# Kernel optimization log

Hardware: AMD Instinct MI355X
Metric: run time of the kernel (lower is better)

Reference implementation:

```python
import jax, jax.numpy as jnp
import numpy as np

N_QUBITS = 10
QLCU_LAYERS = 2
FEATURE_DIM = 256
BATCH = 256
N_PARAMS = 5 * N_QUBITS * QLCU_LAYERS  # 100
TWO_PI = 2.0 * np.pi


def _rx_mat(theta):
    # (B,) -> (B,2,2) complex64
    c = jnp.cos(theta / 2).astype(jnp.complex64)
    s = (-1j * jnp.sin(theta / 2)).astype(jnp.complex64)
    return jnp.stack([jnp.stack([c, s], -1), jnp.stack([s, c], -1)], -2)


def _ry_mat(theta):
    c = jnp.cos(theta / 2).astype(jnp.complex64)
    s = jnp.sin(theta / 2).astype(jnp.complex64)
    return jnp.stack([jnp.stack([c, -s], -1), jnp.stack([s, c], -1)], -2)


def _rz_mat(theta):
    e0 = jnp.exp(-0.5j * theta.astype(jnp.complex64))
    e1 = jnp.exp(0.5j * theta.astype(jnp.complex64))
    z = jnp.zeros_like(e0)
    return jnp.stack([jnp.stack([e0, z], -1), jnp.stack([z, e1], -1)], -2)


def _apply_1q(state, U, w):
    # state: (B,)+(2,)*n ; U: (B,2,2) ; wire w (PennyLane wire 0 = most significant)
    s = jnp.moveaxis(state, 1 + w, -1)
    s = jnp.einsum('bij,b...j->b...i', U, s)
    return jnp.moveaxis(s, -1, 1 + w)


def _apply_crx(state, theta, c, t):
    # controlled-RX: apply RX(theta) on target t where control c == 1
    s = jnp.moveaxis(state, (1 + c, 1 + t), (-2, -1))
    U = _rx_mat(theta)
    s1 = jnp.einsum('bij,b...j->b...i', U, s[..., 1, :])
    s = jnp.stack([s[..., 0, :], s1], axis=-2)
    return jnp.moveaxis(s, (-2, -1), (1 + c, 1 + t))


def _circuit(params):
    # params: (B, N_PARAMS) angles. Returns (B, 3*n) expvals [X.., Y.., Z..]
    n = N_QUBITS
    B = params.shape[0]
    state = jnp.zeros((B,) + (2,) * n, jnp.complex64)
    state = state.at[(slice(None),) + (0,) * n].set(1.0)
    idx = 0
    for _ in range(QLCU_LAYERS):
        for i in range(n):
            state = _apply_1q(state, _rx_mat(params[:, idx]), i)
            state = _apply_1q(state, _ry_mat(params[:, idx + 1]), i)
            state = _apply_1q(state, _rz_mat(params[:, idx + 2]), i)
            idx += 3
        for i in range(n):
            state = _apply_crx(state, params[:, idx], i, (i + 1) % n)
            idx += 1
        for i in range(n - 1, -1, -1):
            state = _apply_crx(state, params[:, idx], i, (i - 1) % n)
            idx += 1
    X, Y, Z = [], [], []
    for w in range(n):
        s = jnp.moveaxis(state, 1 + w, -1).reshape(B, -1, 2)
        z01 = jnp.sum(jnp.conj(s[..., 0]) * s[..., 1], axis=1)  # (B,)
        X.append(2.0 * jnp.real(z01))
        Y.append(2.0 * jnp.imag(z01))
        probs = jnp.sum(jnp.abs(s) ** 2, axis=1)  # (B,2)
        Z.append(probs[:, 0] - probs[:, 1])
    return jnp.stack(X + Y + Z, axis=1).astype(jnp.float32)


def _branch(x, W, b, base):
    p = x @ W.T + b            # (B, N_PARAMS)
    p = p + base[None, :]
    p = jax.nn.sigmoid(p) * TWO_PI
    return _circuit(p)


def setup_inputs() -> dict:
    key = jax.random.key(0)
    ks = jax.random.split(key, 16)
    d = {
        'x': jax.random.normal(ks[0], (BATCH, FEATURE_DIM), jnp.float32),
        'W1': jax.random.normal(ks[1], (N_PARAMS, FEATURE_DIM), jnp.float32) * 0.05,
        'b1': jnp.zeros((N_PARAMS,), jnp.float32),
        'W2': jax.random.normal(ks[2], (N_PARAMS, FEATURE_DIM), jnp.float32) * 0.05,
        'b2': jnp.zeros((N_PARAMS,), jnp.float32),
        'W3': jax.random.normal(ks[3], (N_PARAMS, FEATURE_DIM), jnp.float32) * 0.05,
        'b3': jnp.zeros((N_PARAMS,), jnp.float32),
        'base1': jax.random.uniform(ks[4], (N_PARAMS,), jnp.float32) * TWO_PI,
        'base2': jax.random.uniform(ks[5], (N_PARAMS,), jnp.float32) * TWO_PI,
        'base3': jax.random.uniform(ks[6], (N_PARAMS,), jnp.float32) * TWO_PI,
        'alpha_real': jax.random.uniform(ks[7], (1,), jnp.float32),
        'alpha_imag': jnp.zeros((1,), jnp.float32),
        'beta_real': jax.random.uniform(ks[8], (1,), jnp.float32),
        'beta_imag': jnp.zeros((1,), jnp.float32),
        'gamma_real': jax.random.uniform(ks[9], (1,), jnp.float32),
        'gamma_imag': jnp.zeros((1,), jnp.float32),
    }
    return d


def reference(x, W1, b1, W2, b2, W3, b3, base1, base2, base3,
              alpha_real, alpha_imag, beta_real, beta_imag, gamma_real, gamma_imag):
    m1 = _branch(x, W1, b1, base1)  # (B, 3n)
    m2 = _branch(x, W2, b2, base2)
    m3 = _branch(x, W3, b3, base3)
    norm = jnp.sqrt(alpha_real**2 + alpha_imag**2 + beta_real**2 + beta_imag**2
                    + gamma_real**2 + gamma_imag**2 + 1e-9)
    ar, ai = alpha_real / norm, alpha_imag / norm
    br, bi = beta_real / norm, beta_imag / norm
    gr, gi = gamma_real / norm, gamma_imag / norm
    re = ar * m1 + br * m2 + gr * m3
    im = ai * m1 + bi * m2 + gi * m3
    return jnp.sqrt(re * re + im * im)
```

## Files before the change

kernel.cpp:

```cpp
#include <hip/hip_runtime.h>
#include <math.h>

#define NQ 10
#define NPAR 100
#define FDIM 256
#define BATCH 256
#define NOUT 30
#define TWO_PI_F 6.283185307179586f
#define NSLOT 4


template<int MASK>
__device__ __forceinline__ float lx(float v) {
    if constexpr (MASK == 1) {
        return __int_as_float(__builtin_amdgcn_update_dpp(
            0, __float_as_int(v), 0xB1, 0xF, 0xF, true));
    } else if constexpr (MASK == 2) {
        return __int_as_float(__builtin_amdgcn_update_dpp(
            0, __float_as_int(v), 0x4E, 0xF, 0xF, true));
    } else if constexpr (MASK == 8) {
        return __int_as_float(__builtin_amdgcn_update_dpp(
            0, __float_as_int(v), 0x128, 0xF, 0xF, true));
    } else if constexpr (MASK == 4) {
        return __int_as_float(__builtin_amdgcn_ds_swizzle(__float_as_int(v), 0x101F));
    } else if constexpr (MASK == 16) {
        return __int_as_float(__builtin_amdgcn_ds_swizzle(__float_as_int(v), 0x401F));
    } else {
        return __shfl_xor(v, 32, 64);
    }
}

template<int MASK>
__device__ __forceinline__ float2 lx2(float2 v) {
    return make_float2(lx<MASK>(v.x), lx<MASK>(v.y));
}

__device__ __forceinline__ float2 cmul(float2 a, float2 b) {
    return make_float2(a.x*b.x - a.y*b.y, a.x*b.y + a.y*b.x);
}

struct Ctx {
    int lane;
    int W;
    int ebuf;
    float2 (*ex)[4][NSLOT][64];
};

template<int BC, int BT>
__device__ __forceinline__ void crx(float2 (&st)[NSLOT], Ctx& cx, float c, float s)
{
    if constexpr (BT >= 8) {
        constexpr int tb = BT - 8;
        const int PW = cx.W ^ (1 << tb);
        if constexpr (BC >= 8) {
            const bool ctrl = (cx.W >> (BC - 8)) & 1;
            if (ctrl) {
                #pragma unroll
                for (int a = 0; a < NSLOT; ++a) cx.ex[cx.ebuf][cx.W][a][cx.lane] = st[a];
            }
            __syncthreads();
            if (ctrl) {
                #pragma unroll
                for (int a = 0; a < NSLOT; ++a) {
                    const float2 p = cx.ex[cx.ebuf][PW][a][cx.lane];
                    const float2 m = st[a];
                    st[a] = make_float2(c*m.x + s*p.y, c*m.y - s*p.x);
                }
            }
            cx.ebuf ^= 1;
        } else if constexpr (BC >= 6) {
            constexpr int rc = 1 << (BC - 6);
            #pragma unroll
            for (int a = 0; a < NSLOT; ++a) if (a & rc) cx.ex[cx.ebuf][cx.W][a][cx.lane] = st[a];
            __syncthreads();
            #pragma unroll
            for (int a = 0; a < NSLOT; ++a) if (a & rc) {
                const float2 p = cx.ex[cx.ebuf][PW][a][cx.lane];
                const float2 m = st[a];
                st[a] = make_float2(c*m.x + s*p.y, c*m.y - s*p.x);
            }
            cx.ebuf ^= 1;
        } else {
            #pragma unroll
            for (int a = 0; a < NSLOT; ++a) cx.ex[cx.ebuf][cx.W][a][cx.lane] = st[a];
            __syncthreads();
            const bool act = (cx.lane >> BC) & 1;
            const float cc = act ? c : 1.f, ss = act ? s : 0.f;
            #pragma unroll
            for (int a = 0; a < NSLOT; ++a) {
                const float2 p = cx.ex[cx.ebuf][PW][a][cx.lane];
                const float2 m = st[a];
                st[a] = make_float2(cc*m.x + ss*p.y, cc*m.y - ss*p.x);
            }
            cx.ebuf ^= 1;
        }
    } else if constexpr (BC >= 8) {
        const bool ctrl = (cx.W >> (BC - 8)) & 1;
        if (ctrl) {
            if constexpr (BT >= 6) {
                constexpr int rt = 1 << (BT - 6);
                #pragma unroll
                for (int a = 0; a < NSLOT; ++a) {
                    if (a & rt) continue;
                    const int a1 = a | rt;
                    const float2 A0 = st[a], A1 = st[a1];
                    st[a]  = make_float2(c*A0.x + s*A1.y, c*A0.y - s*A1.x);
                    st[a1] = make_float2(c*A1.x + s*A0.y, c*A1.y - s*A0.x);
                }
            } else {
                constexpr int M = 1 << BT;
                #pragma unroll
                for (int a = 0; a < NSLOT; ++a) {
                    const float2 p = lx2<M>(st[a]); const float2 m = st[a];
                    st[a] = make_float2(c*m.x + s*p.y, c*m.y - s*p.x);
                }
            }
        }
    } else if constexpr (BT >= 6) {
        constexpr int rt = 1 << (BT - 6);
        if constexpr (BC >= 6) {
            constexpr int rc = 1 << (BC - 6);
            #pragma unroll
            for (int a = 0; a < NSLOT; ++a) {
                if (!(a & rc) || (a & rt)) continue;
                const int a1 = a | rt;
                const float2 A0 = st[a], A1 = st[a1];
                st[a]  = make_float2(c*A0.x + s*A1.y, c*A0.y - s*A1.x);
                st[a1] = make_float2(c*A1.x + s*A0.y, c*A1.y - s*A0.x);
            }
        } else {
            const bool act = (cx.lane >> BC) & 1;
            const float cc = act ? c : 1.f, ss = act ? s : 0.f;
            #pragma unroll
            for (int a = 0; a < NSLOT; ++a) {
                if (a & rt) continue;
                const int a1 = a | rt;
                const float2 A0 = st[a], A1 = st[a1];
                st[a]  = make_float2(cc*A0.x + ss*A1.y, cc*A0.y - ss*A1.x);
                st[a1] = make_float2(cc*A1.x + ss*A0.y, cc*A1.y - ss*A0.x);
            }
        }
    } else {
        constexpr int M = 1 << BT;
        if constexpr (BC >= 6) {
            constexpr int rc = 1 << (BC - 6);
            #pragma unroll
            for (int a = 0; a < NSLOT; ++a) {
                if (!(a & rc)) continue;
                const float2 p = lx2<M>(st[a]); const float2 m = st[a];
                st[a] = make_float2(c*m.x + s*p.y, c*m.y - s*p.x);
            }
        } else {
            const bool act = (cx.lane >> BC) & 1;
            const float cc = act ? c : 1.f, ss = act ? s : 0.f;
            #pragma unroll
            for (int a = 0; a < NSLOT; ++a) {
                const float2 p = lx2<M>(st[a]); const float2 m = st[a];
                st[a] = make_float2(cc*m.x + ss*p.y, cc*m.y - ss*p.x);
            }
        }
    }
}

template<int BIT>
__device__ __forceinline__ void gate1q(float2 (&st)[NSLOT], Ctx& cx,
                                       float2 u00, float2 u01, float2 u10, float2 u11)
{
    if constexpr (BIT >= 8) {
        constexpr int tb = BIT - 8;
        const int PW = cx.W ^ (1 << tb);
        #pragma unroll
        for (int a = 0; a < NSLOT; ++a) cx.ex[cx.ebuf][cx.W][a][cx.lane] = st[a];
        __syncthreads();
        const bool hi = (cx.W >> tb) & 1;
        const float2 A = hi ? u11 : u00;
        const float2 B = hi ? u10 : u01;
        #pragma unroll
        for (int a = 0; a < NSLOT; ++a) {
            const float2 m = st[a];
            const float2 p = cx.ex[cx.ebuf][PW][a][cx.lane];
            st[a] = make_float2(A.x*m.x - A.y*m.y + B.x*p.x - B.y*p.y,
                                A.x*m.y + A.y*m.x + B.x*p.y + B.y*p.x);
        }
        cx.ebuf ^= 1;
    } else if constexpr (BIT >= 6) {
        constexpr int rb = 1 << (BIT - 6);
        #pragma unroll
        for (int a = 0; a < NSLOT; ++a) {
            if (a & rb) continue;
            const int a1 = a | rb;
            const float2 A0 = st[a], A1 = st[a1];
            float2 n0, n1;
            n0.x = u00.x*A0.x - u00.y*A0.y + u01.x*A1.x - u01.y*A1.y;
            n0.y = u00.x*A0.y + u00.y*A0.x + u01.x*A1.y + u01.y*A1.x;
            n1.x = u10.x*A0.x - u10.y*A0.y + u11.x*A1.x - u11.y*A1.y;
            n1.y = u10.x*A0.y + u10.y*A0.x + u11.x*A1.y + u11.y*A1.x;
            st[a] = n0; st[a1] = n1;
        }
    } else {
        constexpr int M = 1 << BIT;
        const bool hi = (cx.lane >> BIT) & 1;
        const float2 A = hi ? u11 : u00;
        const float2 B = hi ? u10 : u01;
        #pragma unroll
        for (int a = 0; a < NSLOT; ++a) {
            const float2 p = lx2<M>(st[a]); const float2 m = st[a];
            st[a] = make_float2(A.x*m.x - A.y*m.y + B.x*p.x - B.y*p.y,
                                A.x*m.y + A.y*m.x + B.x*p.y + B.y*p.x);
        }
    }
}

template<int Q>
__device__ __forceinline__ void layer1q(float2 (&st)[NSLOT], Ctx& cx,
                                        const float2* cs, int idx)
{
    if constexpr (Q < NQ) {
        const float2 X = cs[idx], Y = cs[idx + 1], Z = cs[idx + 2];
        const float cx_ = X.x, sx = X.y, cy = Y.x, sy = Y.y, cz = Z.x, sz = Z.y;
        const float2 m00 = make_float2( cy*cx_,  sy*sx);
        const float2 m01 = make_float2(-sy*cx_, -cy*sx);
        const float2 m10 = make_float2( sy*cx_, -cy*sx);
        const float2 m11 = make_float2( cy*cx_, -sy*sx);
        const float2 u00 = make_float2(cz*m00.x + sz*m00.y, cz*m00.y - sz*m00.x);
        const float2 u01 = make_float2(cz*m01.x + sz*m01.y, cz*m01.y - sz*m01.x);
        const float2 u10 = make_float2(cz*m10.x - sz*m10.y, cz*m10.y + sz*m10.x);
        const float2 u11 = make_float2(cz*m11.x - sz*m11.y, cz*m11.y + sz*m11.x);
        gate1q<9 - Q>(st, cx, u00, u01, u10, u11);
        layer1q<Q + 1>(st, cx, cs, idx + 3);
    }
}

template<int Q>
__device__ __forceinline__ void ringF(float2 (&st)[NSLOT], Ctx& cx,
                                      const float2* cs, int idx)
{
    if constexpr (Q < NQ) {
        const float2 p = cs[idx];
        crx<9 - Q, 9 - ((Q + 1) % NQ)>(st, cx, p.x, p.y);
        ringF<Q + 1>(st, cx, cs, idx + 1);
    }
}

template<int Q>
__device__ __forceinline__ void ringB(float2 (&st)[NSLOT], Ctx& cx,
                                      const float2* cs, int idx)
{
    if constexpr (Q >= 0) {
        const float2 p = cs[idx];
        crx<9 - Q, 9 - ((Q + NQ - 1) % NQ)>(st, cx, p.x, p.y);
        ringB<Q - 1>(st, cx, cs, idx + 1);
    }
}

__device__ __forceinline__ void col0(const float2* cs, int w, float2& u00, float2& u10)
{
    const float2 X = cs[3*w], Y = cs[3*w + 1], Z = cs[3*w + 2];
    const float cx = X.x, sx = X.y, cy = Y.x, sy = Y.y, cz = Z.x, sz = Z.y;
    const float2 m00 = make_float2(cy*cx,  sy*sx);
    const float2 m10 = make_float2(sy*cx, -cy*sx);
    u00 = make_float2(cz*m00.x + sz*m00.y, cz*m00.y - sz*m00.x);
    u10 = make_float2(cz*m10.x - sz*m10.y, cz*m10.y + sz*m10.x);
}

template<int Wq>
__device__ __forceinline__ void measureAll(const float2 (&st)[NSLOT], Ctx& cx,
                                           float* mrow )
{
    if constexpr (Wq < NQ) {
        constexpr int B = 9 - Wq;
        float sre = 0.f, smm = 0.f, szz = 0.f;
        if constexpr (B >= 8) {
            constexpr int tb = B - 8;
            const int PW = cx.W ^ (1 << tb);
            #pragma unroll
            for (int a = 0; a < NSLOT; ++a) cx.ex[cx.ebuf][cx.W][a][cx.lane] = st[a];
            __syncthreads();
            const float sgn = ((cx.W >> tb) & 1) ? -1.f : 1.f;
            #pragma unroll
            for (int a = 0; a < NSLOT; ++a) {
                const float2 m = st[a];
                const float2 p = cx.ex[cx.ebuf][PW][a][cx.lane];
                sre += m.x*p.x + m.y*p.y;
                smm += sgn * (m.x*p.y - m.y*p.x);
                szz += sgn * (m.x*m.x + m.y*m.y);
            }
            cx.ebuf ^= 1;
        } else if constexpr (B >= 6) {
            constexpr int rb = 1 << (B - 6);
            #pragma unroll
            for (int a = 0; a < NSLOT; ++a) {
                if (a & rb) continue;
                const int a1 = a | rb;
                const float2 A0 = st[a], A1 = st[a1];
                sre += A0.x*A1.x + A0.y*A1.y;
                smm += A0.x*A1.y - A0.y*A1.x;
                szz += A0.x*A0.x + A0.y*A0.y - A1.x*A1.x - A1.y*A1.y;
            }
            sre *= 2.f; smm *= 2.f;
        } else {
            constexpr int M = 1 << B;
            const float sgn = ((cx.lane >> B) & 1) ? -1.f : 1.f;
            #pragma unroll
            for (int a = 0; a < NSLOT; ++a) {
                const float2 m = st[a];
                const float2 p = lx2<M>(m);
                sre += m.x*p.x + m.y*p.y;
                smm += sgn * (m.x*p.y - m.y*p.x);
                szz += sgn * (m.x*m.x + m.y*m.y - p.x*p.x - p.y*p.y);
            }
            szz *= 0.5f;
        }
        sre += lx<1>(sre); sre += lx<2>(sre); sre += lx<4>(sre); sre += lx<8>(sre); sre += lx<16>(sre);
        smm += lx<1>(smm); smm += lx<2>(smm); smm += lx<4>(smm); smm += lx<8>(smm); smm += lx<16>(smm);
        szz += lx<1>(szz); szz += lx<2>(szz); szz += lx<4>(szz); szz += lx<8>(szz); szz += lx<16>(szz);
        if ((cx.lane & 31) == 0) {
            const int k = (cx.W << 1) | (cx.lane >> 5);
            mrow[k * NOUT + Wq]      = sre;
            mrow[k * NOUT + 10 + Wq] = smm;
            mrow[k * NOUT + 20 + Wq] = szz;
        }
        measureAll<Wq + 1>(st, cx, mrow);
    }
}

__global__ __launch_bounds__(768) void qsb_fused(
    const float* __restrict__ x,
    const float* __restrict__ W1, const float* __restrict__ b1, const float* __restrict__ base1,
    const float* __restrict__ W2, const float* __restrict__ b2, const float* __restrict__ base2,
    const float* __restrict__ W3, const float* __restrict__ b3, const float* __restrict__ base3,
    const float* __restrict__ ar_, const float* __restrict__ ai_,
    const float* __restrict__ br_, const float* __restrict__ bi_,
    const float* __restrict__ gr_, const float* __restrict__ gi_,
    float* __restrict__ out)
{
    const int tid  = threadIdx.x;
    const int b    = blockIdx.x;
    const int wv   = tid >> 6;
    const int br   = wv >> 2;
    const int W    = wv & 3;
    const int lane = tid & 63;
    const int lt   = (W << 6) | lane;

    const float* Wp   = (br == 0) ? W1    : (br == 1) ? W2    : W3;
    const float* bias = (br == 0) ? b1    : (br == 1) ? b2    : b3;
    const float* base = (br == 0) ? base1 : (br == 1) ? base2 : base3;

    __shared__ float2 css[3][NPAR];
    __shared__ float2 exb[3][2][4][NSLOT][64];
    __shared__ float  mred[3][8][NOUT];

    if (lt < NPAR) {
        const float4* xr = reinterpret_cast<const float4*>(x + (size_t)b * FDIM);
        const float4* wr = reinterpret_cast<const float4*>(Wp + (size_t)lt * FDIM);
        float a0 = 0.f, a1 = 0.f, a2 = 0.f, a3 = 0.f;
        #pragma unroll 8
        for (int k = 0; k < FDIM / 4; ++k) {
            const float4 xv = xr[k];
            const float4 wv4 = wr[k];
            a0 += xv.x*wv4.x; a1 += xv.y*wv4.y; a2 += xv.z*wv4.z; a3 += xv.w*wv4.w;
        }
        float acc = (a0 + a1) + (a2 + a3);
        acc += bias[lt] + base[lt];
        const float t = TWO_PI_F / (1.f + __expf(-acc));
        float sn, cn;
        __sincosf(0.5f * t, &sn, &cn);
        css[br][lt] = make_float2(cn, sn);
    }
    __syncthreads();

    const float2* cs = css[br];
    Ctx cx;
    cx.lane = lane; cx.W = W; cx.ebuf = 0;
    cx.ex = exb[br];

    float2 st[NSLOT];
    {
        float2 lp = make_float2(1.f, 0.f);
        #pragma unroll
        for (int bb = 0; bb < 6; ++bb) {
            float2 u00, u10;
            col0(cs, 9 - bb, u00, u10);
            lp = cmul(lp, ((lane >> bb) & 1) ? u10 : u00);
        }
        {
            float2 u00, u10;
            col0(cs, 1, u00, u10);
            lp = cmul(lp, (W & 1) ? u10 : u00);
        }
        {
            float2 u00, u10;
            col0(cs, 0, u00, u10);
            lp = cmul(lp, ((W >> 1) & 1) ? u10 : u00);
        }
        float2 f3[2], f2v[2];
        col0(cs, 3, f3[0], f3[1]);
        col0(cs, 2, f2v[0], f2v[1]);
        #pragma unroll
        for (int a = 0; a < NSLOT; ++a)
            st[a] = cmul(cmul(f3[a & 1], f2v[(a >> 1) & 1]), lp);
    }

    ringF<0>(st, cx, cs, 30);
    ringB<NQ - 1>(st, cx, cs, 40);
    layer1q<0>(st, cx, cs, 50);
    ringF<0>(st, cx, cs, 80);
    ringB<NQ - 1>(st, cx, cs, 90);

    measureAll<0>(st, cx, &mred[br][0][0]);
    __syncthreads();

    if (tid < NOUT) {
        const int j = tid;
        float m1 = 0.f, m2 = 0.f, m3 = 0.f;
        #pragma unroll
        for (int k = 0; k < 8; ++k) {
            m1 += mred[0][k][j];
            m2 += mred[1][k][j];
            m3 += mred[2][k][j];
        }
        const float ar = ar_[0], ai = ai_[0];
        const float brr = br_[0], bii = bi_[0];
        const float gr = gr_[0], gi = gi_[0];
        const float inv = 1.f / sqrtf(ar*ar + ai*ai + brr*brr + bii*bii
                                      + gr*gr + gi*gi + 1e-9f);
        const float re = (ar * m1 + brr * m2 + gr * m3) * inv;
        const float im = (ai * m1 + bii * m2 + gi * m3) * inv;
        out[(size_t)b * NOUT + j] = sqrtf(re * re + im * im);
    }
}

extern "C" void kernel_launch(void* const* d_in, const int* in_sizes, int n_in,
                              void* d_out, int out_size, void* d_ws, size_t ws_size,
                              hipStream_t stream)
{
    (void)in_sizes; (void)n_in; (void)out_size; (void)d_ws; (void)ws_size;
    const float* x     = (const float*)d_in[0];
    const float* W1    = (const float*)d_in[1];
    const float* b1    = (const float*)d_in[2];
    const float* W2    = (const float*)d_in[3];
    const float* b2    = (const float*)d_in[4];
    const float* W3    = (const float*)d_in[5];
    const float* b3    = (const float*)d_in[6];
    const float* base1 = (const float*)d_in[7];
    const float* base2 = (const float*)d_in[8];
    const float* base3 = (const float*)d_in[9];
    const float* ar    = (const float*)d_in[10];
    const float* ai    = (const float*)d_in[11];
    const float* br    = (const float*)d_in[12];
    const float* bi    = (const float*)d_in[13];
    const float* gr    = (const float*)d_in[14];
    const float* gi    = (const float*)d_in[15];

    qsb_fused<<<dim3(BATCH), dim3(768), 0, stream>>>(
        x, W1, b1, base1, W2, b2, base2, W3, b3, base3,
        ar, ai, br, bi, gr, gi, (float*)d_out);
}
```

Baseline: 107.2 us.

## Split fused kernel into per-branch simulation blocks plus a combine kernel

The single 768-thread block per sample, which ran all three branch circuits, becomes three 256-thread blocks per sample, one per branch. Each writes its partial expectation values to workspace, and a second small kernel applies the complex weighting and magnitude. The aim is finer-grained blocks that schedule better across CUs and allow higher occupancy. The cost is an extra kernel launch and a global-memory round trip for the partials.

```diff
diff --git a/kernel.cpp b/kernel.cpp
--- a/kernel.cpp
+++ b/kernel.cpp
@@ -324,35 +324,31 @@
     }
 }
 
-__global__ __launch_bounds__(768) void qsb_fused(
+__global__ __launch_bounds__(256) void qsb_sim(
     const float* __restrict__ x,
     const float* __restrict__ W1, const float* __restrict__ b1, const float* __restrict__ base1,
     const float* __restrict__ W2, const float* __restrict__ b2, const float* __restrict__ base2,
     const float* __restrict__ W3, const float* __restrict__ b3, const float* __restrict__ base3,
-    const float* __restrict__ ar_, const float* __restrict__ ai_,
-    const float* __restrict__ br_, const float* __restrict__ bi_,
-    const float* __restrict__ gr_, const float* __restrict__ gi_,
-    float* __restrict__ out)
-{
+    float* __restrict__ gpart )
+{
+    const int bb   = blockIdx.x;
+    const int b    = bb / 3;
+    const int br   = bb - 3 * b;
     const int tid  = threadIdx.x;
-    const int b    = blockIdx.x;
-    const int wv   = tid >> 6;
-    const int br   = wv >> 2;
-    const int W    = wv & 3;
+    const int W    = tid >> 6;
     const int lane = tid & 63;
-    const int lt   = (W << 6) | lane;
 
     const float* Wp   = (br == 0) ? W1    : (br == 1) ? W2    : W3;
     const float* bias = (br == 0) ? b1    : (br == 1) ? b2    : b3;
     const float* base = (br == 0) ? base1 : (br == 1) ? base2 : base3;
 
-    __shared__ float2 css[3][NPAR];
-    __shared__ float2 exb[3][2][4][NSLOT][64];
-    __shared__ float  mred[3][8][NOUT];
-
-    if (lt < NPAR) {
+    __shared__ float2 css[NPAR];
+    __shared__ float2 exb[2][4][NSLOT][64];
+    __shared__ float  mred[8][NOUT];
+
+    if (tid < NPAR) {
         const float4* xr = reinterpret_cast<const float4*>(x + (size_t)b * FDIM);
-        const float4* wr = reinterpret_cast<const float4*>(Wp + (size_t)lt * FDIM);
+        const float4* wr = reinterpret_cast<const float4*>(Wp + (size_t)tid * FDIM);
         float a0 = 0.f, a1 = 0.f, a2 = 0.f, a3 = 0.f;
         #pragma unroll 8
         for (int k = 0; k < FDIM / 4; ++k) {
@@ -361,27 +357,27 @@
             a0 += xv.x*wv4.x; a1 += xv.y*wv4.y; a2 += xv.z*wv4.z; a3 += xv.w*wv4.w;
         }
         float acc = (a0 + a1) + (a2 + a3);
-        acc += bias[lt] + base[lt];
+        acc += bias[tid] + base[tid];
         const float t = TWO_PI_F / (1.f + __expf(-acc));
         float sn, cn;
         __sincosf(0.5f * t, &sn, &cn);
-        css[br][lt] = make_float2(cn, sn);
+        css[tid] = make_float2(cn, sn);
     }
     __syncthreads();
 
-    const float2* cs = css[br];
+    const float2* cs = css;
     Ctx cx;
     cx.lane = lane; cx.W = W; cx.ebuf = 0;
-    cx.ex = exb[br];
+    cx.ex = exb;
 
     float2 st[NSLOT];
     {
         float2 lp = make_float2(1.f, 0.f);
         #pragma unroll
-        for (int bb = 0; bb < 6; ++bb) {
+        for (int bbit = 0; bbit < 6; ++bbit) {
             float2 u00, u10;
-            col0(cs, 9 - bb, u00, u10);
-            lp = cmul(lp, ((lane >> bb) & 1) ? u10 : u00);
+            col0(cs, 9 - bbit, u00, u10);
+            lp = cmul(lp, ((lane >> bbit) & 1) ? u10 : u00);
         }
         {
             float2 u00, u10;
@@ -407,34 +403,46 @@
     ringF<0>(st, cx, cs, 80);
     ringB<NQ - 1>(st, cx, cs, 90);
 
-    measureAll<0>(st, cx, &mred[br][0][0]);
+    measureAll<0>(st, cx, &mred[0][0]);
     __syncthreads();
 
     if (tid < NOUT) {
-        const int j = tid;
-        float m1 = 0.f, m2 = 0.f, m3 = 0.f;
-        #pragma unroll
-        for (int k = 0; k < 8; ++k) {
-            m1 += mred[0][k][j];
-            m2 += mred[1][k][j];
-            m3 += mred[2][k][j];
-        }
-        const float ar = ar_[0], ai = ai_[0];
-        const float brr = br_[0], bii = bi_[0];
-        const float gr = gr_[0], gi = gi_[0];
-        const float inv = 1.f / sqrtf(ar*ar + ai*ai + brr*brr + bii*bii
-                                      + gr*gr + gi*gi + 1e-9f);
-        const float re = (ar * m1 + brr * m2 + gr * m3) * inv;
-        const float im = (ai * m1 + bii * m2 + gi * m3) * inv;
-        out[(size_t)b * NOUT + j] = sqrtf(re * re + im * im);
-    }
+        float m = 0.f;
+        #pragma unroll
+        for (int k = 0; k < 8; ++k) m += mred[k][tid];
+        gpart[(size_t)bb * NOUT + tid] = m;
+    }
+}
+
+__global__ __launch_bounds__(128) void qsb_combine(
+    const float* __restrict__ gpart,
+    const float* __restrict__ ar_, const float* __restrict__ ai_,
+    const float* __restrict__ br_, const float* __restrict__ bi_,
+    const float* __restrict__ gr_, const float* __restrict__ gi_,
+    float* __restrict__ out)
+{
+    const int idx = blockIdx.x * 128 + threadIdx.x;
+    if (idx >= BATCH * NOUT) return;
+    const int b = idx / NOUT;
+    const int j = idx - b * NOUT;
+    const float m1 = gpart[(size_t)(b * 3 + 0) * NOUT + j];
+    const float m2 = gpart[(size_t)(b * 3 + 1) * NOUT + j];
+    const float m3 = gpart[(size_t)(b * 3 + 2) * NOUT + j];
+    const float ar = ar_[0], ai = ai_[0];
+    const float brr = br_[0], bii = bi_[0];
+    const float gr = gr_[0], gi = gi_[0];
+    const float inv = 1.f / sqrtf(ar*ar + ai*ai + brr*brr + bii*bii
+                                  + gr*gr + gi*gi + 1e-9f);
+    const float re = (ar * m1 + brr * m2 + gr * m3) * inv;
+    const float im = (ai * m1 + bii * m2 + gi * m3) * inv;
+    out[(size_t)b * NOUT + j] = sqrtf(re * re + im * im);
 }
 
 extern "C" void kernel_launch(void* const* d_in, const int* in_sizes, int n_in,
                               void* d_out, int out_size, void* d_ws, size_t ws_size,
                               hipStream_t stream)
 {
-    (void)in_sizes; (void)n_in; (void)out_size; (void)d_ws; (void)ws_size;
+    (void)in_sizes; (void)n_in; (void)out_size; (void)ws_size;
     const float* x     = (const float*)d_in[0];
     const float* W1    = (const float*)d_in[1];
     const float* b1    = (const float*)d_in[2];
@@ -452,7 +460,12 @@
     const float* gr    = (const float*)d_in[14];
     const float* gi    = (const float*)d_in[15];
 
-    qsb_fused<<<dim3(BATCH), dim3(768), 0, stream>>>(
-        x, W1, b1, base1, W2, b2, base2, W3, b3, base3,
-        ar, ai, br, bi, gr, gi, (float*)d_out);
-}
+    float* gpart = (float*)d_ws;
+
+    qsb_sim<<<dim3(BATCH * 3), dim3(256), 0, stream>>>(
+        x, W1, b1, base1, W2, b2, base2, W3, b3, base3, gpart);
+
+    const int total = BATCH * NOUT;
+    qsb_combine<<<dim3((total + 127) / 128), dim3(128), 0, stream>>>(
+        gpart, ar, ai, br, bi, gr, gi, (float*)d_out);
+}
```

After: 109.0 us. Within noise of the previous version (+1.7%).
